# Optimization experiments

Measured on AMD Instinct MI355X. Metric: run time of the kernel, lower is better.

## Reference

```python
import jax, jax.numpy as jnp
import numpy as np

B, C, N, L, K, PRED = 64, 2, 1024, 24, 3, 12


def setup_inputs() -> dict:
    key = jax.random.key(0)
    ks = jax.random.split(key, 32)
    u = lambda k, shape, s: jax.random.uniform(k, shape, jnp.float32, -s, s)
    stdv_gc = 1.0 / np.sqrt(N)
    stdv_g = 1.0 / np.sqrt(N * (K + 1))
    stdv_r = 1.0 / np.sqrt(2 * N)
    inp = {
        'inputs': jax.random.normal(ks[0], (B, C, N, L), jnp.float32),
        'adj': (jax.random.uniform(ks[1], (N, N)) < 0.05).astype(jnp.float32),
        'gc_w': u(ks[2], (K, N, N), stdv_gc),
        'Wf': u(ks[3], (N, N * (K + 1)), stdv_g), 'bf': u(ks[4], (N,), stdv_g),
        'Wi': u(ks[5], (N, N * (K + 1)), stdv_g), 'bi': u(ks[6], (N,), stdv_g),
        'Wo': u(ks[7], (N, N * (K + 1)), stdv_g), 'bo': u(ks[8], (N,), stdv_g),
        'Wc': u(ks[9], (N, N * (K + 1)), stdv_g), 'bc': u(ks[10], (N,), stdv_g),
        'rWf': u(ks[11], (N, 2 * N), stdv_r), 'rbf': u(ks[12], (N,), stdv_r),
        'rWi': u(ks[13], (N, 2 * N), stdv_r), 'rbi': u(ks[14], (N,), stdv_r),
        'rWo': u(ks[15], (N, 2 * N), stdv_r), 'rbo': u(ks[16], (N,), stdv_r),
        'rWc': u(ks[17], (N, 2 * N), stdv_r), 'rbc': u(ks[18], (N,), stdv_r),
        'neighbor_w': u(ks[19], (N,), stdv_gc),
        'c': jnp.ones((1,), jnp.float32),
        'conv_w': u(ks[20], (C * PRED, C), 1.0 / np.sqrt(C)),
        'conv_b': u(ks[21], (C * PRED,), 1.0 / np.sqrt(C)),
    }
    return inp


def _build_A_list(adj, k):
    # tmp = sum(A, 0); zeros -> 1e-5; 'D_inverse' = diag(tmp) (as in original code)
    tmp = jnp.sum(adj, 0)
    tmp = jnp.where(tmp == 0, 1e-5, tmp)
    a_norm = tmp[:, None] * adj  # diag(tmp) @ A
    a_list = []
    a_tmp = jnp.eye(adj.shape[0], dtype=adj.dtype)
    for _ in range(k):
        a_tmp = jnp.minimum(a_tmp @ a_norm, 1.0)  # clamp max=1.0
        a_list.append(a_tmp)
    return a_list


def _forward(adj, inputs, gc_w, Wf, bf, Wi, bi, Wo, bo, Wc, bc,
             rWf, rbf, rWi, rbi, rWo, rbo, rWc, rbc, neighbor_w, c, conv_w, conv_b):
    b, ch, n, l = inputs.shape
    k = gc_w.shape[0]
    a_list = _build_A_list(adj, k)
    a_stack = jnp.stack(a_list)            # (K,N,N)
    eff_w = a_stack * gc_w                 # masked FilterLinear weights
    nbr = a_list[-1] @ neighbor_w          # (N,)
    Wg = jnp.concatenate([Wf, Wi, Wo, Wc], 0)      # fused gate weights (4N, (K+1)N)
    bg = jnp.concatenate([bf, bi, bo, bc], 0)
    rWg = jnp.concatenate([rWf, rWi, rWo, rWc], 0)  # (4N, 2N)
    rbg = jnp.concatenate([rbf, rbi, rbo, rbc], 0)

    def step(carry, x):  # x: (B,C,N)
        H, Cs, rH, rCs, _ = carry
        # gc = cat_k FilterLinear_k(x), each x @ (A_k*W_k)^T
        gc = jnp.einsum('bcn,kmn->bckm', x, eff_w).reshape(b, ch, k * n)
        g = jnp.concatenate([gc, H], -1) @ Wg.T + bg
        f, i, o, Ct = jnp.split(g, 4, -1)
        Cs = jax.nn.sigmoid(f) * (Cs * nbr) + jax.nn.sigmoid(i) * jnp.tanh(Ct)
        H = jax.nn.sigmoid(o) * jnp.tanh(Cs)
        rg = jnp.concatenate([x, rH], -1) @ rWg.T + rbg
        rf, ri, ro, rCt = jnp.split(rg, 4, -1)
        rCs = jax.nn.sigmoid(rf) * rCs + jax.nn.sigmoid(ri) * jnp.tanh(rCt)
        rH = jax.nn.sigmoid(ro) * jnp.tanh(rCs)
        var1 = jnp.var(x, axis=(0, 2), keepdims=True, ddof=1)   # (1,C,1), unbiased like torch
        var2 = jnp.var(gc, axis=(0, 2), keepdims=True, ddof=1)
        pred = (H * var1 * c + rH * var2) / (var1 + var2 * c)
        return (H, Cs, rH, rCs, pred), None

    z = jnp.zeros((b, ch, n), inputs.dtype)
    xs = jnp.moveaxis(inputs, -1, 0)  # (L,B,C,N)
    (H, Cs, rH, rCs, pred), _ = jax.lax.scan(step, (z, z, z, z, z), xs)
    # Conv1d(C, C*pred_len, k=1) then reshape (B,C,N,pred_len)
    out = jnp.einsum('bcn,oc->bon', pred, conv_w) + conv_b[:, None]
    return out.reshape(b, ch, n, -1)


def reference(inputs, adj, gc_w, Wf, bf, Wi, bi, Wo, bo, Wc, bc,
              rWf, rbf, rWi, rbi, rWo, rbo, rWc, rbc, neighbor_w, c, conv_w, conv_b):
    return _forward(adj, inputs, gc_w, Wf, bf, Wi, bi, Wo, bo, Wc, bc,
                    rWf, rbf, rWi, rbi, rWo, rbo, rWc, rbc, neighbor_w, c, conv_w, conv_b)
```

## Files before the change

kernel.cpp:

```cpp
#include <hip/hip_runtime.h>
#include <cmath>

#define NN 1024
#define BC 128
#define LS 24

typedef unsigned short u16;
typedef __attribute__((ext_vector_type(4))) float f32x4;
typedef __attribute__((ext_vector_type(8))) short bf16x8;
typedef __attribute__((ext_vector_type(8))) unsigned short u16x8;

typedef __attribute__((address_space(1))) const void* as1cv;
typedef __attribute__((address_space(3))) void* as3v;

#define GLD16(gp, lp) __builtin_amdgcn_global_load_lds((as1cv)(gp), (as3v)(lp), 16, 0, 0)

__device__ __forceinline__ float sigf(float x){ return 1.0f/(1.0f+expf(-x)); }

__device__ __forceinline__ u16 f2b(float x){
  union { float f; unsigned u; } v; v.f = x;
  unsigned r = v.u + 0x7FFFu + ((v.u >> 16) & 1u);
  return (u16)(r >> 16);
}
__device__ __forceinline__ float b2f(u16 b){
  union { unsigned u; float f; } v; v.u = ((unsigned)b) << 16;
  return v.f;
}

__global__ void k_prep(const float* __restrict__ inputs, const float* __restrict__ adj,
                       const float* __restrict__ Wf, const float* __restrict__ Wi,
                       const float* __restrict__ Wo, const float* __restrict__ Wc,
                       const float* __restrict__ rWf, const float* __restrict__ rWi,
                       const float* __restrict__ rWo, const float* __restrict__ rWc,
                       const float* __restrict__ bf_, const float* __restrict__ bi_,
                       const float* __restrict__ bo_, const float* __restrict__ bc_,
                       const float* __restrict__ rbf, const float* __restrict__ rbi,
                       const float* __restrict__ rbo, const float* __restrict__ rbc,
                       u16* __restrict__ Xb, float* __restrict__ csum,
                       u16* __restrict__ Wgxb, u16* __restrict__ WgHp,
                       u16* __restrict__ rWgxb, u16* __restrict__ rWgHp,
                       float* __restrict__ bgcat){
  int b = blockIdx.x, tid = threadIdx.x;
  if (b < 512){
    int idx = b*256 + tid;
    const float4* p = (const float4*)(inputs + (size_t)idx*LS);
    float v[LS];
    #pragma unroll
    for (int q = 0; q < 6; ++q){
      float4 f = p[q];
      v[q*4]=f.x; v[q*4+1]=f.y; v[q*4+2]=f.z; v[q*4+3]=f.w;
    }
    #pragma unroll
    for (int t = 0; t < LS; ++t)
      Xb[(size_t)t*BC*NN + idx] = f2b(v[t]);
  } else if (b < 576){
    int bb = b - 512;
    for (int j = tid; j < 1024; j += 256){
      float s = 0.f;
      for (int i = 0; i < 16; ++i) s += adj[(size_t)(bb*16+i)*1024 + j];
      csum[(size_t)bb*1024 + j] = s;
    }
  } else if (b < 592){
    int idx = (b-576)*256 + tid;
    int seg = idx >> 10, j = idx & 1023;
    bgcat[idx]      = (seg==0?bf_: seg==1?bi_: seg==2?bo_:bc_)[j];
    bgcat[4096+idx] = (seg==0?rbf: seg==1?rbi: seg==2?rbo:rbc)[j];
  } else {
    int idx = (b-592)*256 + tid;
    if (idx < 2097152){
      int kg = idx & 511, r = idx >> 9;
      int seg = r >> 10, j = r & 1023;
      const float* W = (seg==0?Wf: seg==1?Wi: seg==2?Wo:Wc) + (size_t)j*4096 + kg*8;
      float4 a = *(const float4*)W;
      float4 c = *(const float4*)(W + 4);
      u16x8 o = { f2b(a.x), f2b(a.y), f2b(a.z), f2b(a.w),
                  f2b(c.x), f2b(c.y), f2b(c.z), f2b(c.w) };
      if (kg < 384) *(u16x8*)(Wgxb + (size_t)r*3072 + kg*8) = o;
      else {
        int p = (j>>3)*32 + seg*8 + (j&7);
        *(u16x8*)(WgHp + (size_t)p*1024 + (kg*8 - 3072)) = o;
      }
    } else {
      int g2 = idx - 2097152;
      int kg = g2 & 255, r = g2 >> 8;
      int seg = r >> 10, j = r & 1023;
      const float* W = (seg==0?rWf: seg==1?rWi: seg==2?rWo:rWc) + (size_t)j*2048 + kg*8;
      float4 a = *(const float4*)W;
      float4 c = *(const float4*)(W + 4);
      u16x8 o = { f2b(a.x), f2b(a.y), f2b(a.z), f2b(a.w),
                  f2b(c.x), f2b(c.y), f2b(c.z), f2b(c.w) };
      if (kg < 128) *(u16x8*)(rWgxb + (size_t)r*1024 + kg*8) = o;
      else {
        int p = (j>>3)*32 + seg*8 + (j&7);
        *(u16x8*)(rWgHp + (size_t)p*1024 + (kg*8 - 1024)) = o;
      }
    }
  }
}

__global__ void k_colsum2(const float* __restrict__ part, float* __restrict__ tmp){
  int j = blockIdx.x*256 + threadIdx.x;
  float s = 0.f;
  for (int b = 0; b < 64; ++b) s += part[(size_t)b*1024 + j];
  tmp[j] = (s == 0.f) ? 1e-5f : s;
}

__global__ void k_anormT(const float* __restrict__ adj, const float* __restrict__ tmp,
                         u16* __restrict__ A1b, u16* __restrict__ anormT){
  __shared__ u16 t[64][65];
  int bi = blockIdx.y*64, bj = blockIdx.x*64;
  for (int e = threadIdx.x; e < 4096; e += 256){
    int r = e >> 6, cc = e & 63;
    float v = tmp[bi+r]*adj[(size_t)(bi+r)*1024 + bj+cc];
    A1b[(size_t)(bi+r)*1024 + bj+cc] = f2b(fminf(v, 1.f));
    t[r][cc] = f2b(v);
  }
  __syncthreads();
  for (int e = threadIdx.x; e < 4096; e += 256){
    int r = e >> 6, cc = e & 63;
    anormT[(size_t)(bj+r)*1024 + bi+cc] = t[cc][r];
  }
}

__global__ void k_nbr(const u16* __restrict__ A3b, const float* __restrict__ nw,
                      float* __restrict__ nbr){
  __shared__ float red[256];
  int row = blockIdx.x;
  float s = 0.f;
  for (int j = threadIdx.x; j < 1024; j += 256)
    s += b2f(A3b[(size_t)row*1024 + j])*nw[j];
  red[threadIdx.x] = s; __syncthreads();
  for (int st = 128; st > 0; st >>= 1){
    if (threadIdx.x < st) red[threadIdx.x] += red[threadIdx.x+st];
    __syncthreads();
  }
  if (threadIdx.x == 0) nbr[row] = red[0];
}

__global__ void k_effT(const u16* __restrict__ Ap, const float* __restrict__ gcw,
                       u16* __restrict__ effb, u16* __restrict__ effbT){
  __shared__ u16 t[64][65];
  int bi = blockIdx.y*64, bj = blockIdx.x*64;
  for (int e = threadIdx.x; e < 4096; e += 256){
    int r = e >> 6, cc = e & 63;
    size_t idx = (size_t)(bi+r)*1024 + bj+cc;
    u16 v = f2b(b2f(Ap[idx]) * gcw[idx]);
    effb[idx] = v;
    t[r][cc] = v;
  }
  __syncthreads();
  for (int e = threadIdx.x; e < 4096; e += 256){
    int r = e >> 6, cc = e & 63;
    effbT[(size_t)(bj+r)*3072 + bi+cc] = t[cc][r];
  }
}

__device__ __forceinline__ void mfma_tile(
    const u16* __restrict__ A, const u16* __restrict__ Bw, int K,
    const float* __restrict__ bias,
    float* __restrict__ outf, u16* __restrict__ outb, int ldc,
    u16* ldsA, u16* ldsB)
{
  const int tid  = threadIdx.x;
  const int lane = tid & 63;
  const int w    = tid >> 6;
  const int wr   = (w >> 1) * 64;
  const int wc   = (w & 1) * 64;
  f32x4 acc[4][4] = {};

  const int lrow = lane >> 3;
  const int srck = ((lane & 7) ^ lrow) * 8;
  for (int k0 = 0; k0 < K; k0 += 64){
    #pragma unroll
    for (int c = 0; c < 4; ++c){
      int row = w*32 + c*8;
      GLD16(A  + (size_t)(row + lrow)*K + k0 + srck, &ldsA[row*64]);
      GLD16(Bw + (size_t)(row + lrow)*K + k0 + srck, &ldsB[row*64]);
    }
    __syncthreads();
    #pragma unroll
    for (int kk = 0; kk < 2; ++kk) {
      bf16x8 af[4], bfr[4];
      #pragma unroll
      for (int mi = 0; mi < 4; ++mi) {
        int row = wr + mi*16 + (lane & 15);
        int grp = (kk*4 + (lane >> 4)) ^ (row & 7);
        af[mi] = *(const bf16x8*)&ldsA[row*64 + grp*8];
      }
      #pragma unroll
      for (int ni = 0; ni < 4; ++ni) {
        int row = wc + ni*16 + (lane & 15);
        int grp = (kk*4 + (lane >> 4)) ^ (row & 7);
        bfr[ni] = *(const bf16x8*)&ldsB[row*64 + grp*8];
      }
      #pragma unroll
      for (int mi = 0; mi < 4; ++mi)
        #pragma unroll
        for (int ni = 0; ni < 4; ++ni)
          acc[mi][ni] = __builtin_amdgcn_mfma_f32_16x16x32_bf16(af[mi], bfr[ni], acc[mi][ni], 0, 0, 0);
    }
    __syncthreads();
  }
  #pragma unroll
  for (int mi = 0; mi < 4; ++mi) {
    #pragma unroll
    for (int ni = 0; ni < 4; ++ni) {
      int col = wc + ni*16 + (lane & 15);
      #pragma unroll
      for (int q = 0; q < 4; ++q) {
        int row = wr + mi*16 + (lane >> 4)*4 + q;
        float v = acc[mi][ni][q];
        if (bias) v += bias[col];
        if (outf) outf[(size_t)row*ldc + col] = v;
        if (outb) outb[(size_t)row*ldc + col] = f2b(v);
      }
    }
  }
}

__global__ __launch_bounds__(256) void k_mfma_pre(
    const u16* __restrict__ Xb, const u16* __restrict__ Bcat,
    const float* __restrict__ bgcat, u16* __restrict__ prebuf)
{
  __shared__ u16 lds[16384];
  int id = blockIdx.y*64 + blockIdx.x;
  int bx = (id & 7)*8 + ((id >> 3) & 7);
  int by = id >> 6;
  mfma_tile(Xb + (size_t)by*128*1024, Bcat + (size_t)bx*128*1024, 1024,
            bgcat + bx*128, nullptr,
            prebuf + (size_t)by*128*8192 + bx*128, 8192,
            lds, lds + 8192);
}

__global__ __launch_bounds__(256) void k_mfma64(
    const u16* __restrict__ Ag, const u16* __restrict__ Bg, int K,
    int clamp1, int swz, u16* __restrict__ outb, int ldc)
{
  __shared__ u16 ldsA[64*128];
  __shared__ u16 ldsB[64*128];
  const int tid  = threadIdx.x;
  const int lane = tid & 63;
  const int w    = tid >> 6;
  const int wr   = (w >> 1) * 32;
  const int wc   = (w & 1) * 32;
  int bx = blockIdx.x, by = blockIdx.y;
  if (swz){
    int id = by*16 + bx;
    by = (id & 7)*8 + ((id >> 3) & 7);
    bx = id >> 6;
  }
  const u16* A = Ag + (size_t)by*64*K;
  const u16* B = Bg + (size_t)bx*64*K;
  f32x4 acc[2][2] = {};

  const int r4  = lane >> 4;
  const int g16 = lane & 15;
  for (int k0 = 0; k0 < K; k0 += 128){
    #pragma unroll
    for (int c = 0; c < 4; ++c){
      int rowb = w*16 + c*4;
      int row = rowb + r4;
      int srcg = (g16 & 8) | ((g16 & 7) ^ (row & 7));
      GLD16(A + (size_t)row*K + k0 + srcg*8, &ldsA[rowb*128]);
      GLD16(B + (size_t)row*K + k0 + srcg*8, &ldsB[rowb*128]);
    }
    __syncthreads();
    #pragma unroll
    for (int kk = 0; kk < 4; ++kk){
      int idx = kk*4 + (lane >> 4);
      bf16x8 af[2], bfr[2];
      #pragma unroll
      for (int mi = 0; mi < 2; ++mi){
        int row = wr + mi*16 + (lane & 15);
        int pa = (idx & 8) | ((idx & 7) ^ (row & 7));
        af[mi] = *(const bf16x8*)&ldsA[row*128 + pa*8];
      }
      #pragma unroll
      for (int ni = 0; ni < 2; ++ni){
        int row = wc + ni*16 + (lane & 15);
        int pb = (idx & 8) | ((idx & 7) ^ (row & 7));
        bfr[ni] = *(const bf16x8*)&ldsB[row*128 + pb*8];
      }
      #pragma unroll
      for (int mi = 0; mi < 2; ++mi)
        #pragma unroll
        for (int ni = 0; ni < 2; ++ni)
          acc[mi][ni] = __builtin_amdgcn_mfma_f32_16x16x32_bf16(af[mi], bfr[ni], acc[mi][ni], 0, 0, 0);
    }
    __syncthreads();
  }
  #pragma unroll
  for (int mi = 0; mi < 2; ++mi){
    #pragma unroll
    for (int ni = 0; ni < 2; ++ni){
      int col = bx*64 + wc + ni*16 + (lane & 15);
      #pragma unroll
      for (int q = 0; q < 4; ++q){
        int row = by*64 + wr + mi*16 + (lane >> 4)*4 + q;
        float v = acc[mi][ni][q];
        if (clamp1) v = fminf(v, 1.f);
        outb[(size_t)row*ldc + col] = f2b(v);
      }
    }
  }
}

__global__ __launch_bounds__(256) void k_step(
    const u16* __restrict__ WgHp, const u16* __restrict__ rWgHp,
    const u16* __restrict__ pre_t,
    const float* __restrict__ nbrv,
    u16* __restrict__ Hb2, u16* __restrict__ rHb2,
    float* __restrict__ Cs, float* __restrict__ rCs,
    float* __restrict__ Hf, float* __restrict__ rHf,
    int ph, int last)
{
  __shared__ u16 ldsA[2][64*128];
  __shared__ u16 ldsB[2][32*128];

  const int tid  = threadIdx.x;
  const int lane = tid & 63;
  const int w    = tid >> 6;
  const int bid  = blockIdx.x;
  const int job  = bid >> 8;
  const int rem  = bid & 255;
  const int s    = rem >> 1;
  const int r0   = (rem & 1) * 64;

  const u16* Bp   = (job ? rWgHp : WgHp) + (size_t)s*32*1024;
  const u16* Ab   = (job ? rHb2 : Hb2) + (size_t)ph*BC*NN + (size_t)r0*NN;
  const u16* pret = pre_t + (size_t)job*4096;
  u16* Hnext  = (job ? rHb2 : Hb2) + (size_t)(ph^1)*BC*NN;
  float* Csb  = job ? rCs : Cs;
  float* Hfin = job ? rHf : Hf;

  const int r4  = lane >> 4;
  const int g16 = lane & 15;

  auto STAGE = [&](int ck, int buf){
    int k0 = ck*128;
    #pragma unroll
    for (int c = 0; c < 4; ++c){
      int rowb = w*16 + c*4;
      int row = rowb + r4;
      int srcg = (g16 & 8) | ((g16 & 7) ^ (row & 7));
      GLD16(Ab + (size_t)row*1024 + k0 + srcg*8, &ldsA[buf][rowb*128]);
    }
    #pragma unroll
    for (int c = 0; c < 2; ++c){
      int rowb = w*8 + c*4;
      int row = rowb + r4;
      int srcg = (g16 & 8) | ((g16 & 7) ^ (row & 7));
      GLD16(Bp + (size_t)row*1024 + k0 + srcg*8, &ldsB[buf][rowb*128]);
    }
  };

  f32x4 acc[2] = {};
  STAGE(0, 0);
  #pragma unroll
  for (int t = 0; t < 8; ++t){
    const int cur = t & 1;
    if (t < 7){
      STAGE(t+1, cur^1);
      asm volatile("s_waitcnt vmcnt(6)" ::: "memory");
    } else {
      asm volatile("s_waitcnt vmcnt(0)" ::: "memory");
    }
    __builtin_amdgcn_sched_barrier(0);
    __builtin_amdgcn_s_barrier();
    #pragma unroll
    for (int kk = 0; kk < 4; ++kk){
      int idx = kk*4 + (lane >> 4);
      int rowa = w*16 + (lane & 15);
      int pa = (idx & 8) | ((idx & 7) ^ (rowa & 7));
      bf16x8 af = *(const bf16x8*)&ldsA[cur][rowa*128 + pa*8];
      #pragma unroll
      for (int ni = 0; ni < 2; ++ni){
        int rowb2 = ni*16 + (lane & 15);
        int pb = (idx & 8) | ((idx & 7) ^ (rowb2 & 7));
        bf16x8 bv = *(const bf16x8*)&ldsB[cur][rowb2*128 + pb*8];
        acc[ni] = __builtin_amdgcn_mfma_f32_16x16x32_bf16(af, bv, acc[ni], 0, 0, 0);
      }
    }
    __builtin_amdgcn_sched_barrier(0);
    __builtin_amdgcn_s_barrier();
  }

  #pragma unroll
  for (int ni = 0; ni < 2; ++ni){
    int pcol = ni*16 + (lane & 15);
    int gcol = (pcol >> 3)*1024 + s*8 + (pcol & 7);
    #pragma unroll
    for (int q = 0; q < 4; ++q){
      int row = r0 + w*16 + (lane >> 4)*4 + q;
      acc[ni][q] += b2f(pret[(size_t)row*8192 + gcol]);
    }
  }
  const bool act = (lane & 15) < 8;
  const int  c   = lane & 7;
  const int  col = s*8 + c;
  float fac = 1.f;
  if (!job && act) fac = nbrv[col];
  #pragma unroll
  for (int q = 0; q < 4; ++q){
    float a0 = acc[0][q], a1 = acc[1][q];
    float p1 = __shfl_xor(a0, 8);
    float p3 = __shfl_xor(a1, 8);
    if (act){
      int row = r0 + w*16 + (lane >> 4)*4 + q;
      float fg = sigf(a0), ig = sigf(p1), og = sigf(a1), ct = tanhf(p3);
      size_t cidx = (size_t)row*NN + col;
      float cs = fg*Csb[cidx]*fac + ig*ct;
      Csb[cidx] = cs;
      float h = og*tanhf(cs);
      Hnext[cidx] = f2b(h);
      if (last) Hfin[cidx] = h;
    }
  }
}

__global__ void k_var1(const u16* __restrict__ Xl, const u16* __restrict__ gcl,
                       float* __restrict__ part){
  int ch = blockIdx.x & 1, seg = blockIdx.x >> 1;
  int tid = threadIdx.x;
  float s1=0.f,q1=0.f,s2=0.f,q2=0.f;
  for (int bb = 0; bb < 2; ++bb){
    int row = (seg*2+bb)*2 + ch;
    const u16* xr = Xl + (size_t)row*1024;
    for (int n = tid; n < 1024; n += 256){ float v = b2f(xr[n]); s1 += v; q1 += v*v; }
    const u16* gr = gcl + (size_t)row*3072;
    for (int n = tid; n < 3072; n += 256){ float v = b2f(gr[n]); s2 += v; q2 += v*v; }
  }
  __shared__ float red[256][4];
  red[tid][0]=s1; red[tid][1]=q1; red[tid][2]=s2; red[tid][3]=q2;
  __syncthreads();
  for (int st = 128; st > 0; st >>= 1){
    if (tid < st){ for (int z = 0; z < 4; ++z) red[tid][z] += red[tid+st][z]; }
    __syncthreads();
  }
  if (tid == 0){ for (int z = 0; z < 4; ++z) part[(size_t)blockIdx.x*4 + z] = red[0][z]; }
}

__global__ void k_out(const float* __restrict__ H, const float* __restrict__ rH,
                      const float* __restrict__ part, const float* __restrict__ cptr,
                      const float* __restrict__ cw, const float* __restrict__ cb,
                      float* __restrict__ out){
  __shared__ float vsh[4];
  int tid = threadIdx.x;
  if (tid < 4){
    int ch = tid & 1, which = tid >> 1;
    float s = 0.f, q = 0.f;
    for (int seg = 0; seg < 32; ++seg){
      const float* p = part + (size_t)(seg*2+ch)*4 + which*2;
      s += p[0]; q += p[1];
    }
    float n = which ? 196608.f : 65536.f;
    vsh[tid] = (q - s*s/n) / (n - 1.f);
  }
  __syncthreads();
  int idx = blockIdx.x*256 + tid;
  int n = idx & 1023, b = idx >> 10;
  float c0 = cptr[0];
  float v10 = vsh[0], v11 = vsh[1], v20 = vsh[2], v21 = vsh[3];
  size_t i0 = (size_t)(b*2+0)*1024 + n, i1 = (size_t)(b*2+1)*1024 + n;
  float p0 = (H[i0]*v10*c0 + rH[i0]*v20) / (v10 + v20*c0);
  float p1 = (H[i1]*v11*c0 + rH[i1]*v21) / (v11 + v21*c0);
  float* ob = out + (size_t)b*24*1024 + n;
  #pragma unroll
  for (int o = 0; o < 24; ++o)
    ob[(size_t)o*1024] = p0*cw[o*2+0] + p1*cw[o*2+1] + cb[o];
}

extern "C" void kernel_launch(void* const* d_in, const int* in_sizes, int n_in,
                              void* d_out, int out_size, void* d_ws, size_t ws_size,
                              hipStream_t stream) {
  const float* inputs = (const float*)d_in[0];
  const float* adj    = (const float*)d_in[1];
  const float* gcw    = (const float*)d_in[2];
  const float* Wf  = (const float*)d_in[3];  const float* bf_ = (const float*)d_in[4];
  const float* Wi  = (const float*)d_in[5];  const float* bi_ = (const float*)d_in[6];
  const float* Wo  = (const float*)d_in[7];  const float* bo_ = (const float*)d_in[8];
  const float* Wc  = (const float*)d_in[9];  const float* bc_ = (const float*)d_in[10];
  const float* rWf = (const float*)d_in[11]; const float* rbf = (const float*)d_in[12];
  const float* rWi = (const float*)d_in[13]; const float* rbi = (const float*)d_in[14];
  const float* rWo = (const float*)d_in[15]; const float* rbo = (const float*)d_in[16];
  const float* rWc = (const float*)d_in[17]; const float* rbc = (const float*)d_in[18];
  const float* nw     = (const float*)d_in[19];
  const float* cscal  = (const float*)d_in[20];
  const float* convw  = (const float*)d_in[21];
  const float* convb  = (const float*)d_in[22];
  float* out = (float*)d_out;

  char* cur = (char*)d_ws;
  auto alloc = [&](size_t bytes) -> void* {
    void* p = cur; cur += (bytes + 255) & ~(size_t)255; return p;
  };
  u16*   Xb     = (u16*)  alloc((size_t)LS*BC*NN*2);
  float* csum   = (float*)alloc((size_t)64*1024*4);
  float* tmpv   = (float*)alloc(1024*4);
  u16*   anormT = (u16*)  alloc((size_t)NN*NN*2);
  u16*   Apowb  = (u16*)  alloc((size_t)3*NN*NN*2);
  float* nbrv   = (float*)alloc(1024*4);
  u16*   effb   = (u16*)  alloc((size_t)3*NN*NN*2);
  u16*   effbT  = (u16*)  alloc((size_t)3*NN*NN*2);
  u16*   Wgxb   = (u16*)  alloc((size_t)4096*3072*2);
  u16*   WgHp   = (u16*)  alloc((size_t)4096*1024*2);
  u16*   rWgHp  = (u16*)  alloc((size_t)4096*1024*2);
  u16*   Bcat   = (u16*)  alloc((size_t)8192*1024*2);
  float* bgcat  = (float*)alloc(8192*4);
  u16*   gclb   = (u16*)  alloc((size_t)BC*3072*2);
  u16*   prebuf = (u16*)  alloc((size_t)3072*8192*2);
  char*  zbase  = cur;
  u16*   Hb2    = (u16*)  alloc((size_t)2*BC*NN*2);
  u16*   rHb2   = (u16*)  alloc((size_t)2*BC*NN*2);
  float* Cs     = (float*)alloc((size_t)BC*NN*4);
  float* rCs    = (float*)alloc((size_t)BC*NN*4);
  size_t zlen   = (size_t)(cur - zbase);
  float* Hfv    = (float*)alloc((size_t)BC*NN*4);
  float* rHfv   = (float*)alloc((size_t)BC*NN*4);
  float* part   = (float*)alloc(64*4*4);

  u16* A1b = Apowb;
  u16* A2b = Apowb + (size_t)NN*NN;
  u16* A3b = Apowb + (size_t)2*NN*NN;
  u16* Cwb   = Bcat;
  u16* rWgxb = Bcat + (size_t)4096*1024;

  k_prep<<<592 + (2097152+1048576)/256, 256, 0, stream>>>(
      inputs, adj, Wf, Wi, Wo, Wc, rWf, rWi, rWo, rWc,
      bf_, bi_, bo_, bc_, rbf, rbi, rbo, rbc,
      Xb, csum, Wgxb, WgHp, rWgxb, rWgHp, bgcat);
  k_colsum2<<<4, 256, 0, stream>>>(csum, tmpv);
  dim3 g16(16, 16);
  k_anormT<<<g16, 256, 0, stream>>>(adj, tmpv, A1b, anormT);
  k_mfma64<<<g16, 256, 0, stream>>>(A1b, anormT, 1024, 1, 0, A2b, 1024);
  k_mfma64<<<g16, 256, 0, stream>>>(A2b, anormT, 1024, 1, 0, A3b, 1024);
  k_nbr<<<NN, 256, 0, stream>>>(A3b, nw, nbrv);
  dim3 geff(16, 48);
  k_effT<<<geff, 256, 0, stream>>>(Apowb, gcw, effb, effbT);

  dim3 gcwg(16, 64);
  k_mfma64<<<gcwg, 256, 0, stream>>>(Wgxb, effbT, 3072, 0, 1, Cwb, 1024);
  dim3 gpre(64, 24);
  k_mfma_pre<<<gpre, 256, 0, stream>>>(Xb, Bcat, bgcat, prebuf);
  dim3 ggcl(48, 2);
  k_mfma64<<<ggcl, 256, 0, stream>>>(Xb + (size_t)(LS-1)*BC*NN, effb, 1024, 0, 0, gclb, 3072);

  hipMemsetAsync(zbase, 0, zlen, stream);

  for (int t = 0; t < LS; ++t)
    k_step<<<512, 256, 0, stream>>>(WgHp, rWgHp,
        prebuf + (size_t)t*BC*8192,
        nbrv, Hb2, rHb2, Cs, rCs, Hfv, rHfv, t & 1, t == LS-1);

  k_var1<<<64, 256, 0, stream>>>(Xb + (size_t)(LS-1)*BC*NN, gclb, part);
  k_out<<<(64*1024)/256, 256, 0, stream>>>(Hfv, rHfv, part, cscal, convw, convb, out);
}
```

Baseline: 529.3 us.

## Fuse recurrent steps into one persistent kernel with grid barrier

```diff
diff --git a/kernel.cpp b/kernel.cpp
--- a/kernel.cpp
+++ b/kernel.cpp
@@ -4,6 +4,7 @@
 #define NN 1024
 #define BC 128
 #define LS 24
+#define LOOPBLK 256
 
 typedef unsigned short u16;
 typedef __attribute__((ext_vector_type(4))) float f32x4;
@@ -305,116 +306,147 @@
   }
 }
 
-__global__ __launch_bounds__(256) void k_step(
+__global__ __launch_bounds__(256) void k_loop(
     const u16* __restrict__ WgHp, const u16* __restrict__ rWgHp,
-    const u16* __restrict__ pre_t,
+    const u16* __restrict__ prebuf,
     const float* __restrict__ nbrv,
     u16* __restrict__ Hb2, u16* __restrict__ rHb2,
-    float* __restrict__ Cs, float* __restrict__ rCs,
     float* __restrict__ Hf, float* __restrict__ rHf,
-    int ph, int last)
+    int* __restrict__ bar)
 {
-  __shared__ u16 ldsA[2][64*128];
-  __shared__ u16 ldsB[2][32*128];
+  __shared__ u16 ldsB[32*1024];
+  __shared__ u16 ldsA[2][128*128];
 
   const int tid  = threadIdx.x;
   const int lane = tid & 63;
   const int w    = tid >> 6;
   const int bid  = blockIdx.x;
-  const int job  = bid >> 8;
-  const int rem  = bid & 255;
-  const int s    = rem >> 1;
-  const int r0   = (rem & 1) * 64;
+  const int job  = bid >> 7;
+  const int s    = bid & 127;
 
   const u16* Bp   = (job ? rWgHp : WgHp) + (size_t)s*32*1024;
-  const u16* Ab   = (job ? rHb2 : Hb2) + (size_t)ph*BC*NN + (size_t)r0*NN;
-  const u16* pret = pre_t + (size_t)job*4096;
-  u16* Hnext  = (job ? rHb2 : Hb2) + (size_t)(ph^1)*BC*NN;
-  float* Csb  = job ? rCs : Cs;
-  float* Hfin = job ? rHf : Hf;
+  const u16* Hsrc = job ? rHb2 : Hb2;
+  u16* Hdst       = job ? rHb2 : Hb2;
+  float* Hfin     = job ? rHf : Hf;
+  const u16* pre0 = prebuf + (size_t)job*4096;
 
   const int r4  = lane >> 4;
   const int g16 = lane & 15;
 
-  auto STAGE = [&](int ck, int buf){
-    int k0 = ck*128;
-    #pragma unroll
-    for (int c = 0; c < 4; ++c){
-      int rowb = w*16 + c*4;
-      int row = rowb + r4;
-      int srcg = (g16 & 8) | ((g16 & 7) ^ (row & 7));
-      GLD16(Ab + (size_t)row*1024 + k0 + srcg*8, &ldsA[buf][rowb*128]);
-    }
+  #pragma unroll
+  for (int ck = 0; ck < 8; ++ck){
     #pragma unroll
     for (int c = 0; c < 2; ++c){
       int rowb = w*8 + c*4;
       int row = rowb + r4;
       int srcg = (g16 & 8) | ((g16 & 7) ^ (row & 7));
-      GLD16(Bp + (size_t)row*1024 + k0 + srcg*8, &ldsB[buf][rowb*128]);
-    }
-  };
-
-  f32x4 acc[2] = {};
-  STAGE(0, 0);
-  #pragma unroll
-  for (int t = 0; t < 8; ++t){
-    const int cur = t & 1;
-    if (t < 7){
-      STAGE(t+1, cur^1);
-      asm volatile("s_waitcnt vmcnt(6)" ::: "memory");
-    } else {
-      asm volatile("s_waitcnt vmcnt(0)" ::: "memory");
-    }
-    __builtin_amdgcn_sched_barrier(0);
-    __builtin_amdgcn_s_barrier();
-    #pragma unroll
-    for (int kk = 0; kk < 4; ++kk){
-      int idx = kk*4 + (lane >> 4);
-      int rowa = w*16 + (lane & 15);
-      int pa = (idx & 8) | ((idx & 7) ^ (rowa & 7));
-      bf16x8 af = *(const bf16x8*)&ldsA[cur][rowa*128 + pa*8];
-      #pragma unroll
-      for (int ni = 0; ni < 2; ++ni){
-        int rowb2 = ni*16 + (lane & 15);
-        int pb = (idx & 8) | ((idx & 7) ^ (rowb2 & 7));
-        bf16x8 bv = *(const bf16x8*)&ldsB[cur][rowb2*128 + pb*8];
-        acc[ni] = __builtin_amdgcn_mfma_f32_16x16x32_bf16(af, bv, acc[ni], 0, 0, 0);
-      }
-    }
-    __builtin_amdgcn_sched_barrier(0);
-    __builtin_amdgcn_s_barrier();
-  }
-
-  #pragma unroll
-  for (int ni = 0; ni < 2; ++ni){
-    int pcol = ni*16 + (lane & 15);
-    int gcol = (pcol >> 3)*1024 + s*8 + (pcol & 7);
-    #pragma unroll
-    for (int q = 0; q < 4; ++q){
-      int row = r0 + w*16 + (lane >> 4)*4 + q;
-      acc[ni][q] += b2f(pret[(size_t)row*8192 + gcol]);
-    }
-  }
+      GLD16(Bp + (size_t)row*1024 + ck*128 + srcg*8, &ldsB[(ck*32 + rowb)*128]);
+    }
+  }
+
   const bool act = (lane & 15) < 8;
   const int  c   = lane & 7;
   const int  col = s*8 + c;
   float fac = 1.f;
   if (!job && act) fac = nbrv[col];
-  #pragma unroll
-  for (int q = 0; q < 4; ++q){
-    float a0 = acc[0][q], a1 = acc[1][q];
-    float p1 = __shfl_xor(a0, 8);
-    float p3 = __shfl_xor(a1, 8);
-    if (act){
-      int row = r0 + w*16 + (lane >> 4)*4 + q;
-      float fg = sigf(a0), ig = sigf(p1), og = sigf(a1), ct = tanhf(p3);
-      size_t cidx = (size_t)row*NN + col;
-      float cs = fg*Csb[cidx]*fac + ig*ct;
-      Csb[cidx] = cs;
-      float h = og*tanhf(cs);
-      Hnext[cidx] = f2b(h);
-      if (last) Hfin[cidx] = h;
-    }
+  float csr[2][4] = {};
+
+  asm volatile("s_waitcnt vmcnt(0)" ::: "memory");
+  __syncthreads();
+
+  for (int t = 0; t < LS; ++t){
+    const int ph = t & 1;
+    const u16* Ab   = Hsrc + (size_t)ph*BC*NN;
+    const u16* pret = pre0 + (size_t)t*BC*8192;
+    u16* Hnext      = Hdst + (size_t)(ph^1)*BC*NN;
+
+    float preld[2][2][4];
+    #pragma unroll
+    for (int mi = 0; mi < 2; ++mi)
+      #pragma unroll
+      for (int ni = 0; ni < 2; ++ni){
+        int pcol = ni*16 + (lane & 15);
+        int gcol = (pcol >> 3)*1024 + s*8 + (pcol & 7);
+        #pragma unroll
+        for (int q = 0; q < 4; ++q){
+          int row = w*32 + mi*16 + (lane >> 4)*4 + q;
+          preld[mi][ni][q] = b2f(pret[(size_t)row*8192 + gcol]);
+        }
+      }
+
+    auto STAGEA = [&](int ck, int buf){
+      int k0 = ck*128;
+      #pragma unroll
+      for (int cc = 0; cc < 8; ++cc){
+        int rowb = w*32 + cc*4;
+        int row = rowb + r4;
+        int srcg = (g16 & 8) | ((g16 & 7) ^ (row & 7));
+        GLD16(Ab + (size_t)row*1024 + k0 + srcg*8, &ldsA[buf][rowb*128]);
+      }
+    };
+
+    f32x4 acc[2][2] = {};
+    STAGEA(0, 0);
+    #pragma unroll
+    for (int ck = 0; ck < 8; ++ck){
+      const int cur = ck & 1;
+      if (ck < 7){
+        STAGEA(ck+1, cur^1);
+        asm volatile("s_waitcnt vmcnt(8)" ::: "memory");
+      } else {
+        asm volatile("s_waitcnt vmcnt(0)" ::: "memory");
+      }
+      __builtin_amdgcn_sched_barrier(0);
+      __builtin_amdgcn_s_barrier();
+      #pragma unroll
+      for (int kk = 0; kk < 4; ++kk){
+        int idx = kk*4 + (lane >> 4);
+        #pragma unroll
+        for (int mi = 0; mi < 2; ++mi){
+          int rowa = w*32 + mi*16 + (lane & 15);
+          int pa = (idx & 8) | ((idx & 7) ^ (rowa & 7));
+          bf16x8 af = *(const bf16x8*)&ldsA[cur][rowa*128 + pa*8];
+          #pragma unroll
+          for (int ni = 0; ni < 2; ++ni){
+            int rowb2 = ni*16 + (lane & 15);
+            int pb = (idx & 8) | ((idx & 7) ^ (rowb2 & 7));
+            bf16x8 bv = *(const bf16x8*)&ldsB[(ck*32 + rowb2)*128 + pb*8];
+            acc[mi][ni] = __builtin_amdgcn_mfma_f32_16x16x32_bf16(af, bv, acc[mi][ni], 0, 0, 0);
+          }
+        }
+      }
+      __builtin_amdgcn_sched_barrier(0);
+      __builtin_amdgcn_s_barrier();
+    }
+
+    #pragma unroll
+    for (int mi = 0; mi < 2; ++mi){
+      #pragma unroll
+      for (int q = 0; q < 4; ++q){
+        float a0 = acc[mi][0][q] + preld[mi][0][q];
+        float a1 = acc[mi][1][q] + preld[mi][1][q];
+        float p1 = __shfl_xor(a0, 8);
+        float p3 = __shfl_xor(a1, 8);
+        if (act){
+          int row = w*32 + mi*16 + (lane >> 4)*4 + q;
+          float fg = sigf(a0), ig = sigf(p1), og = sigf(a1), ct = tanhf(p3);
+          float cs = fg*csr[mi][q]*fac + ig*ct;
+          csr[mi][q] = cs;
+          float h = og*tanhf(cs);
+          Hnext[(size_t)row*NN + col] = f2b(h);
+          if (t == LS-1) Hfin[(size_t)row*NN + col] = h;
+        }
+      }
+    }
+
+    __threadfence();
+    __syncthreads();
+    if (tid == 0){
+      atomicAdd(&bar[t], 1);
+      while (__hip_atomic_load(&bar[t], __ATOMIC_RELAXED, __HIP_MEMORY_SCOPE_AGENT) < LOOPBLK) {}
+    }
+    __syncthreads();
+    __threadfence();
   }
 }
 
@@ -512,8 +544,7 @@
   char*  zbase  = cur;
   u16*   Hb2    = (u16*)  alloc((size_t)2*BC*NN*2);
   u16*   rHb2   = (u16*)  alloc((size_t)2*BC*NN*2);
-  float* Cs     = (float*)alloc((size_t)BC*NN*4);
-  float* rCs    = (float*)alloc((size_t)BC*NN*4);
+  int*   bar    = (int*)  alloc(LS*4);
   size_t zlen   = (size_t)(cur - zbase);
   float* Hfv    = (float*)alloc((size_t)BC*NN*4);
   float* rHfv   = (float*)alloc((size_t)BC*NN*4);
@@ -547,10 +578,8 @@
 
   hipMemsetAsync(zbase, 0, zlen, stream);
 
-  for (int t = 0; t < LS; ++t)
-    k_step<<<512, 256, 0, stream>>>(WgHp, rWgHp,
-        prebuf + (size_t)t*BC*8192,
-        nbrv, Hb2, rHb2, Cs, rCs, Hfv, rHfv, t & 1, t == LS-1);
+  k_loop<<<LOOPBLK, 256, 0, stream>>>(WgHp, rWgHp, prebuf, nbrv,
+                                      Hb2, rHb2, Hfv, rHfv, bar);
 
   k_var1<<<64, 256, 0, stream>>>(Xb + (size_t)(LS-1)*BC*NN, gclb, part);
   k_out<<<(64*1024)/256, 256, 0, stream>>>(Hfv, rHfv, part, cscal, convw, convb, out);
```

Result: slower. 1.541 ms (+191.2%).

## Merge small prep kernels and widen recurrent step tiles to 512 threads

Applied to the files above, without the earlier changes.

```diff
diff --git a/kernel.cpp b/kernel.cpp
--- a/kernel.cpp
+++ b/kernel.cpp
@@ -122,36 +122,39 @@
   }
 }
 
-__global__ void k_nbr(const u16* __restrict__ A3b, const float* __restrict__ nw,
-                      float* __restrict__ nbr){
+__global__ void k_nbreff(const u16* __restrict__ A3b, const float* __restrict__ nw,
+                         float* __restrict__ nbr,
+                         const u16* __restrict__ Ap, const float* __restrict__ gcw,
+                         u16* __restrict__ effb, u16* __restrict__ effbT){
   __shared__ float red[256];
-  int row = blockIdx.x;
-  float s = 0.f;
-  for (int j = threadIdx.x; j < 1024; j += 256)
-    s += b2f(A3b[(size_t)row*1024 + j])*nw[j];
-  red[threadIdx.x] = s; __syncthreads();
-  for (int st = 128; st > 0; st >>= 1){
-    if (threadIdx.x < st) red[threadIdx.x] += red[threadIdx.x+st];
+  __shared__ u16 t[64][65];
+  int b = blockIdx.x, tid = threadIdx.x;
+  if (b < 1024){
+    int row = b;
+    float s = 0.f;
+    for (int j = tid; j < 1024; j += 256)
+      s += b2f(A3b[(size_t)row*1024 + j])*nw[j];
+    red[tid] = s; __syncthreads();
+    for (int st = 128; st > 0; st >>= 1){
+      if (tid < st) red[tid] += red[tid+st];
+      __syncthreads();
+    }
+    if (tid == 0) nbr[row] = red[0];
+  } else {
+    int e2 = b - 1024;
+    int bj = (e2 & 15)*64, bi = (e2 >> 4)*64;
+    for (int e = tid; e < 4096; e += 256){
+      int r = e >> 6, cc = e & 63;
+      size_t idx = (size_t)(bi+r)*1024 + bj+cc;
+      u16 v = f2b(b2f(Ap[idx]) * gcw[idx]);
+      effb[idx] = v;
+      t[r][cc] = v;
+    }
     __syncthreads();
-  }
-  if (threadIdx.x == 0) nbr[row] = red[0];
-}
-
-__global__ void k_effT(const u16* __restrict__ Ap, const float* __restrict__ gcw,
-                       u16* __restrict__ effb, u16* __restrict__ effbT){
-  __shared__ u16 t[64][65];
-  int bi = blockIdx.y*64, bj = blockIdx.x*64;
-  for (int e = threadIdx.x; e < 4096; e += 256){
-    int r = e >> 6, cc = e & 63;
-    size_t idx = (size_t)(bi+r)*1024 + bj+cc;
-    u16 v = f2b(b2f(Ap[idx]) * gcw[idx]);
-    effb[idx] = v;
-    t[r][cc] = v;
-  }
-  __syncthreads();
-  for (int e = threadIdx.x; e < 4096; e += 256){
-    int r = e >> 6, cc = e & 63;
-    effbT[(size_t)(bj+r)*3072 + bi+cc] = t[cc][r];
+    for (int e = tid; e < 4096; e += 256){
+      int r = e >> 6, cc = e & 63;
+      effbT[(size_t)(bj+r)*3072 + bi+cc] = t[cc][r];
+    }
   }
 }
 
@@ -220,16 +223,26 @@
 
 __global__ __launch_bounds__(256) void k_mfma_pre(
     const u16* __restrict__ Xb, const u16* __restrict__ Bcat,
-    const float* __restrict__ bgcat, u16* __restrict__ prebuf)
+    const float* __restrict__ bgcat, u16* __restrict__ prebuf,
+    const u16* __restrict__ Xlast, const u16* __restrict__ effb,
+    u16* __restrict__ gclb)
 {
   __shared__ u16 lds[16384];
-  int id = blockIdx.y*64 + blockIdx.x;
-  int bx = (id & 7)*8 + ((id >> 3) & 7);
-  int by = id >> 6;
-  mfma_tile(Xb + (size_t)by*128*1024, Bcat + (size_t)bx*128*1024, 1024,
-            bgcat + bx*128, nullptr,
-            prebuf + (size_t)by*128*8192 + bx*128, 8192,
-            lds, lds + 8192);
+  int id = blockIdx.x;
+  if (id < 1536){
+    int bx = (id & 7)*8 + ((id >> 3) & 7);
+    int by = id >> 6;
+    mfma_tile(Xb + (size_t)by*128*1024, Bcat + (size_t)bx*128*1024, 1024,
+              bgcat + bx*128, nullptr,
+              prebuf + (size_t)by*128*8192 + bx*128, 8192,
+              lds, lds + 8192);
+  } else {
+    int g = id - 1536;
+    mfma_tile(Xlast, effb + (size_t)g*128*1024, 1024,
+              nullptr, nullptr,
+              gclb + (size_t)g*128, 3072,
+              lds, lds + 8192);
+  }
 }
 
 __global__ __launch_bounds__(256) void k_mfma64(
@@ -305,7 +318,7 @@
   }
 }
 
-__global__ __launch_bounds__(256) void k_step(
+__global__ __launch_bounds__(512) void k_step(
     const u16* __restrict__ WgHp, const u16* __restrict__ rWgHp,
     const u16* __restrict__ pre_t,
     const float* __restrict__ nbrv,
@@ -315,18 +328,20 @@
     int ph, int last)
 {
   __shared__ u16 ldsA[2][64*128];
-  __shared__ u16 ldsB[2][32*128];
+  __shared__ u16 ldsB[2][64*128];
 
   const int tid  = threadIdx.x;
   const int lane = tid & 63;
   const int w    = tid >> 6;
+  const int mw   = w >> 1;
+  const int nh   = w & 1;
   const int bid  = blockIdx.x;
-  const int job  = bid >> 8;
-  const int rem  = bid & 255;
-  const int s    = rem >> 1;
+  const int job  = bid >> 7;
+  const int rem  = bid & 127;
+  const int p    = rem >> 1;
   const int r0   = (rem & 1) * 64;
 
-  const u16* Bp   = (job ? rWgHp : WgHp) + (size_t)s*32*1024;
+  const u16* Bp   = (job ? rWgHp : WgHp) + (size_t)p*64*1024;
   const u16* Ab   = (job ? rHb2 : Hb2) + (size_t)ph*BC*NN + (size_t)r0*NN;
   const u16* pret = pre_t + (size_t)job*4096;
   u16* Hnext  = (job ? rHb2 : Hb2) + (size_t)(ph^1)*BC*NN;
@@ -339,17 +354,11 @@
   auto STAGE = [&](int ck, int buf){
     int k0 = ck*128;
     #pragma unroll
-    for (int c = 0; c < 4; ++c){
-      int rowb = w*16 + c*4;
-      int row = rowb + r4;
-      int srcg = (g16 & 8) | ((g16 & 7) ^ (row & 7));
-      GLD16(Ab + (size_t)row*1024 + k0 + srcg*8, &ldsA[buf][rowb*128]);
-    }
-    #pragma unroll
     for (int c = 0; c < 2; ++c){
       int rowb = w*8 + c*4;
       int row = rowb + r4;
       int srcg = (g16 & 8) | ((g16 & 7) ^ (row & 7));
+      GLD16(Ab + (size_t)row*1024 + k0 + srcg*8, &ldsA[buf][rowb*128]);
       GLD16(Bp + (size_t)row*1024 + k0 + srcg*8, &ldsB[buf][rowb*128]);
     }
   };
@@ -361,7 +370,7 @@
     const int cur = t & 1;
     if (t < 7){
       STAGE(t+1, cur^1);
-      asm volatile("s_waitcnt vmcnt(6)" ::: "memory");
+      asm volatile("s_waitcnt vmcnt(4)" ::: "memory");
     } else {
       asm volatile("s_waitcnt vmcnt(0)" ::: "memory");
     }
@@ -370,12 +379,12 @@
     #pragma unroll
     for (int kk = 0; kk < 4; ++kk){
       int idx = kk*4 + (lane >> 4);
-      int rowa = w*16 + (lane & 15);
+      int rowa = mw*16 + (lane & 15);
       int pa = (idx & 8) | ((idx & 7) ^ (rowa & 7));
       bf16x8 af = *(const bf16x8*)&ldsA[cur][rowa*128 + pa*8];
       #pragma unroll
       for (int ni = 0; ni < 2; ++ni){
-        int rowb2 = ni*16 + (lane & 15);
+        int rowb2 = nh*32 + ni*16 + (lane & 15);
         int pb = (idx & 8) | ((idx & 7) ^ (rowb2 & 7));
         bf16x8 bv = *(const bf16x8*)&ldsB[cur][rowb2*128 + pb*8];
         acc[ni] = __builtin_amdgcn_mfma_f32_16x16x32_bf16(af, bv, acc[ni], 0, 0, 0);
@@ -385,29 +394,22 @@
     __builtin_amdgcn_s_barrier();
   }
 
-  #pragma unroll
-  for (int ni = 0; ni < 2; ++ni){
-    int pcol = ni*16 + (lane & 15);
-    int gcol = (pcol >> 3)*1024 + s*8 + (pcol & 7);
-    #pragma unroll
-    for (int q = 0; q < 4; ++q){
-      int row = r0 + w*16 + (lane >> 4)*4 + q;
-      acc[ni][q] += b2f(pret[(size_t)row*8192 + gcol]);
-    }
-  }
+  const int b8 = (lane & 15) >> 3;
+  const int gcol0 = (0*2 + b8)*1024 + (2*p + nh)*8 + (lane & 7);
+  const int gcol1 = (1*2 + b8)*1024 + (2*p + nh)*8 + (lane & 7);
   const bool act = (lane & 15) < 8;
-  const int  c   = lane & 7;
-  const int  col = s*8 + c;
+  const int  col = p*16 + nh*8 + (lane & 7);
   float fac = 1.f;
   if (!job && act) fac = nbrv[col];
   #pragma unroll
   for (int q = 0; q < 4; ++q){
-    float a0 = acc[0][q], a1 = acc[1][q];
-    float p1 = __shfl_xor(a0, 8);
-    float p3 = __shfl_xor(a1, 8);
+    int row = r0 + mw*16 + (lane >> 4)*4 + q;
+    float a0 = acc[0][q] + b2f(pret[(size_t)row*8192 + gcol0]);
+    float a1 = acc[1][q] + b2f(pret[(size_t)row*8192 + gcol1]);
+    float vi  = __shfl_xor(a0, 8);
+    float vct = __shfl_xor(a1, 8);
     if (act){
-      int row = r0 + w*16 + (lane >> 4)*4 + q;
-      float fg = sigf(a0), ig = sigf(p1), og = sigf(a1), ct = tanhf(p3);
+      float fg = sigf(a0), ig = sigf(vi), og = sigf(a1), ct = tanhf(vct);
       size_t cidx = (size_t)row*NN + col;
       float cs = fg*Csb[cidx]*fac + ig*ct;
       Csb[cidx] = cs;
@@ -529,26 +531,21 @@
       inputs, adj, Wf, Wi, Wo, Wc, rWf, rWi, rWo, rWc,
       bf_, bi_, bo_, bc_, rbf, rbi, rbo, rbc,
       Xb, csum, Wgxb, WgHp, rWgxb, rWgHp, bgcat);
+  hipMemsetAsync(zbase, 0, zlen, stream);
   k_colsum2<<<4, 256, 0, stream>>>(csum, tmpv);
   dim3 g16(16, 16);
   k_anormT<<<g16, 256, 0, stream>>>(adj, tmpv, A1b, anormT);
   k_mfma64<<<g16, 256, 0, stream>>>(A1b, anormT, 1024, 1, 0, A2b, 1024);
   k_mfma64<<<g16, 256, 0, stream>>>(A2b, anormT, 1024, 1, 0, A3b, 1024);
-  k_nbr<<<NN, 256, 0, stream>>>(A3b, nw, nbrv);
-  dim3 geff(16, 48);
-  k_effT<<<geff, 256, 0, stream>>>(Apowb, gcw, effb, effbT);
+  k_nbreff<<<1792, 256, 0, stream>>>(A3b, nw, nbrv, Apowb, gcw, effb, effbT);
 
   dim3 gcwg(16, 64);
   k_mfma64<<<gcwg, 256, 0, stream>>>(Wgxb, effbT, 3072, 0, 1, Cwb, 1024);
-  dim3 gpre(64, 24);
-  k_mfma_pre<<<gpre, 256, 0, stream>>>(Xb, Bcat, bgcat, prebuf);
-  dim3 ggcl(48, 2);
-  k_mfma64<<<ggcl, 256, 0, stream>>>(Xb + (size_t)(LS-1)*BC*NN, effb, 1024, 0, 0, gclb, 3072);
-
-  hipMemsetAsync(zbase, 0, zlen, stream);
+  k_mfma_pre<<<1560, 256, 0, stream>>>(Xb, Bcat, bgcat, prebuf,
+                                       Xb + (size_t)(LS-1)*BC*NN, effb, gclb);
 
   for (int t = 0; t < LS; ++t)
-    k_step<<<512, 256, 0, stream>>>(WgHp, rWgHp,
+    k_step<<<256, 512, 0, stream>>>(WgHp, rWgHp,
         prebuf + (size_t)t*BC*8192,
         nbrv, Hb2, rHb2, Cs, rCs, Hfv, rHfv, t & 1, t == LS-1);
 
```

Result: no change. 539.3 us (+1.9%).

## Fold per-timestep input projection GEMM into recurrent step kernel launches

Applied to the files above, without the earlier changes.

```diff
diff --git a/kernel.cpp b/kernel.cpp
--- a/kernel.cpp
+++ b/kernel.cpp
@@ -155,81 +155,80 @@
   }
 }
 
-__device__ __forceinline__ void mfma_tile(
-    const u16* __restrict__ A, const u16* __restrict__ Bw, int K,
-    const float* __restrict__ bias,
-    float* __restrict__ outf, u16* __restrict__ outb, int ldc,
-    u16* ldsA, u16* ldsB)
+__device__ __forceinline__ void pre_tile64(int g, const u16* __restrict__ Xs,
+                                           const u16* __restrict__ Bcat,
+                                           const float* __restrict__ bgcat,
+                                           u16* __restrict__ outs, u16* lds)
 {
+  u16* ldsA = lds;
+  u16* ldsB = lds + 8192;
   const int tid  = threadIdx.x;
   const int lane = tid & 63;
   const int w    = tid >> 6;
-  const int wr   = (w >> 1) * 64;
-  const int wc   = (w & 1) * 64;
-  f32x4 acc[4][4] = {};
-
-  const int lrow = lane >> 3;
-  const int srck = ((lane & 7) ^ lrow) * 8;
-  for (int k0 = 0; k0 < K; k0 += 64){
+  const int wr   = (w >> 1) * 32;
+  const int wc   = (w & 1) * 32;
+  const int rh = g >> 7, cp = g & 127;
+  const u16* A = Xs + (size_t)rh*64*1024;
+  const u16* B = Bcat + (size_t)cp*64*1024;
+  f32x4 acc[2][2] = {};
+
+  const int r4  = lane >> 4;
+  const int g16 = lane & 15;
+  for (int k0 = 0; k0 < 1024; k0 += 128){
     #pragma unroll
     for (int c = 0; c < 4; ++c){
-      int row = w*32 + c*8;
-      GLD16(A  + (size_t)(row + lrow)*K + k0 + srck, &ldsA[row*64]);
-      GLD16(Bw + (size_t)(row + lrow)*K + k0 + srck, &ldsB[row*64]);
+      int rowb = w*16 + c*4;
+      int row = rowb + r4;
+      int srcg = (g16 & 8) | ((g16 & 7) ^ (row & 7));
+      GLD16(A + (size_t)row*1024 + k0 + srcg*8, &ldsA[rowb*128]);
+      GLD16(B + (size_t)row*1024 + k0 + srcg*8, &ldsB[rowb*128]);
     }
     __syncthreads();
     #pragma unroll
-    for (int kk = 0; kk < 2; ++kk) {
-      bf16x8 af[4], bfr[4];
-      #pragma unroll
-      for (int mi = 0; mi < 4; ++mi) {
+    for (int kk = 0; kk < 4; ++kk){
+      int idx = kk*4 + (lane >> 4);
+      bf16x8 af[2], bfr[2];
+      #pragma unroll
+      for (int mi = 0; mi < 2; ++mi){
         int row = wr + mi*16 + (lane & 15);
-        int grp = (kk*4 + (lane >> 4)) ^ (row & 7);
-        af[mi] = *(const bf16x8*)&ldsA[row*64 + grp*8];
-      }
-      #pragma unroll
-      for (int ni = 0; ni < 4; ++ni) {
+        int pa = (idx & 8) | ((idx & 7) ^ (row & 7));
+        af[mi] = *(const bf16x8*)&ldsA[row*128 + pa*8];
+      }
+      #pragma unroll
+      for (int ni = 0; ni < 2; ++ni){
         int row = wc + ni*16 + (lane & 15);
-        int grp = (kk*4 + (lane >> 4)) ^ (row & 7);
-        bfr[ni] = *(const bf16x8*)&ldsB[row*64 + grp*8];
-      }
-      #pragma unroll
-      for (int mi = 0; mi < 4; ++mi)
+        int pb = (idx & 8) | ((idx & 7) ^ (row & 7));
+        bfr[ni] = *(const bf16x8*)&ldsB[row*128 + pb*8];
+      }
+      #pragma unroll
+      for (int mi = 0; mi < 2; ++mi)
         #pragma unroll
-        for (int ni = 0; ni < 4; ++ni)
+        for (int ni = 0; ni < 2; ++ni)
           acc[mi][ni] = __builtin_amdgcn_mfma_f32_16x16x32_bf16(af[mi], bfr[ni], acc[mi][ni], 0, 0, 0);
     }
     __syncthreads();
   }
   #pragma unroll
-  for (int mi = 0; mi < 4; ++mi) {
-    #pragma unroll
-    for (int ni = 0; ni < 4; ++ni) {
-      int col = wc + ni*16 + (lane & 15);
-      #pragma unroll
-      for (int q = 0; q < 4; ++q) {
-        int row = wr + mi*16 + (lane >> 4)*4 + q;
-        float v = acc[mi][ni][q];
-        if (bias) v += bias[col];
-        if (outf) outf[(size_t)row*ldc + col] = v;
-        if (outb) outb[(size_t)row*ldc + col] = f2b(v);
-      }
-    }
-  }
-}
-
-__global__ __launch_bounds__(256) void k_mfma_pre(
-    const u16* __restrict__ Xb, const u16* __restrict__ Bcat,
-    const float* __restrict__ bgcat, u16* __restrict__ prebuf)
+  for (int mi = 0; mi < 2; ++mi){
+    #pragma unroll
+    for (int ni = 0; ni < 2; ++ni){
+      int col = cp*64 + wc + ni*16 + (lane & 15);
+      float bv = bgcat[col];
+      #pragma unroll
+      for (int q = 0; q < 4; ++q){
+        int row = rh*64 + wr + mi*16 + (lane >> 4)*4 + q;
+        outs[(size_t)row*8192 + col] = f2b(acc[mi][ni][q] + bv);
+      }
+    }
+  }
+}
+
+__global__ __launch_bounds__(256) void k_pre0(
+    const u16* __restrict__ Xs, const u16* __restrict__ Bcat,
+    const float* __restrict__ bgcat, u16* __restrict__ outs)
 {
   __shared__ u16 lds[16384];
-  int id = blockIdx.y*64 + blockIdx.x;
-  int bx = (id & 7)*8 + ((id >> 3) & 7);
-  int by = id >> 6;
-  mfma_tile(Xb + (size_t)by*128*1024, Bcat + (size_t)bx*128*1024, 1024,
-            bgcat + bx*128, nullptr,
-            prebuf + (size_t)by*128*8192 + bx*128, 8192,
-            lds, lds + 8192);
+  pre_tile64(blockIdx.x, Xs, Bcat, bgcat, outs, lds);
 }
 
 __global__ __launch_bounds__(256) void k_mfma64(
@@ -308,19 +307,29 @@
 __global__ __launch_bounds__(256) void k_step(
     const u16* __restrict__ WgHp, const u16* __restrict__ rWgHp,
     const u16* __restrict__ pre_t,
+    const u16* __restrict__ Xb_next, const u16* __restrict__ Bcat,
+    const float* __restrict__ bgcat, u16* __restrict__ pre_next, int do_pre,
     const float* __restrict__ nbrv,
     u16* __restrict__ Hb2, u16* __restrict__ rHb2,
     float* __restrict__ Cs, float* __restrict__ rCs,
     float* __restrict__ Hf, float* __restrict__ rHf,
     int ph, int last)
 {
-  __shared__ u16 ldsA[2][64*128];
-  __shared__ u16 ldsB[2][32*128];
+  __shared__ u16 lds[24576];
 
   const int tid  = threadIdx.x;
   const int lane = tid & 63;
   const int w    = tid >> 6;
   const int bid  = blockIdx.x;
+
+  if (bid >= 512){
+    if (do_pre) pre_tile64(bid - 512, Xb_next, Bcat, bgcat, pre_next, lds);
+    return;
+  }
+
+  u16* ldsA0 = lds;
+  u16* ldsB0 = lds + 16384;
+
   const int job  = bid >> 8;
   const int rem  = bid & 255;
   const int s    = rem >> 1;
@@ -343,14 +352,14 @@
       int rowb = w*16 + c*4;
       int row = rowb + r4;
       int srcg = (g16 & 8) | ((g16 & 7) ^ (row & 7));
-      GLD16(Ab + (size_t)row*1024 + k0 + srcg*8, &ldsA[buf][rowb*128]);
+      GLD16(Ab + (size_t)row*1024 + k0 + srcg*8, &ldsA0[buf*8192 + rowb*128]);
     }
     #pragma unroll
     for (int c = 0; c < 2; ++c){
       int rowb = w*8 + c*4;
       int row = rowb + r4;
       int srcg = (g16 & 8) | ((g16 & 7) ^ (row & 7));
-      GLD16(Bp + (size_t)row*1024 + k0 + srcg*8, &ldsB[buf][rowb*128]);
+      GLD16(Bp + (size_t)row*1024 + k0 + srcg*8, &ldsB0[buf*4096 + rowb*128]);
     }
   };
 
@@ -372,12 +381,12 @@
       int idx = kk*4 + (lane >> 4);
       int rowa = w*16 + (lane & 15);
       int pa = (idx & 8) | ((idx & 7) ^ (rowa & 7));
-      bf16x8 af = *(const bf16x8*)&ldsA[cur][rowa*128 + pa*8];
+      bf16x8 af = *(const bf16x8*)&ldsA0[cur*8192 + rowa*128 + pa*8];
       #pragma unroll
       for (int ni = 0; ni < 2; ++ni){
         int rowb2 = ni*16 + (lane & 15);
         int pb = (idx & 8) | ((idx & 7) ^ (rowb2 & 7));
-        bf16x8 bv = *(const bf16x8*)&ldsB[cur][rowb2*128 + pb*8];
+        bf16x8 bv = *(const bf16x8*)&ldsB0[cur*4096 + rowb2*128 + pb*8];
         acc[ni] = __builtin_amdgcn_mfma_f32_16x16x32_bf16(af, bv, acc[ni], 0, 0, 0);
       }
     }
@@ -529,6 +538,7 @@
       inputs, adj, Wf, Wi, Wo, Wc, rWf, rWi, rWo, rWc,
       bf_, bi_, bo_, bc_, rbf, rbi, rbo, rbc,
       Xb, csum, Wgxb, WgHp, rWgxb, rWgHp, bgcat);
+  hipMemsetAsync(zbase, 0, zlen, stream);
   k_colsum2<<<4, 256, 0, stream>>>(csum, tmpv);
   dim3 g16(16, 16);
   k_anormT<<<g16, 256, 0, stream>>>(adj, tmpv, A1b, anormT);
@@ -540,17 +550,18 @@
 
   dim3 gcwg(16, 64);
   k_mfma64<<<gcwg, 256, 0, stream>>>(Wgxb, effbT, 3072, 0, 1, Cwb, 1024);
-  dim3 gpre(64, 24);
-  k_mfma_pre<<<gpre, 256, 0, stream>>>(Xb, Bcat, bgcat, prebuf);
+  k_pre0<<<256, 256, 0, stream>>>(Xb, Bcat, bgcat, prebuf);
   dim3 ggcl(48, 2);
   k_mfma64<<<ggcl, 256, 0, stream>>>(Xb + (size_t)(LS-1)*BC*NN, effb, 1024, 0, 0, gclb, 3072);
 
-  hipMemsetAsync(zbase, 0, zlen, stream);
-
-  for (int t = 0; t < LS; ++t)
-    k_step<<<512, 256, 0, stream>>>(WgHp, rWgHp,
+  for (int t = 0; t < LS; ++t){
+    int tn = (t+1 < LS) ? t+1 : t;
+    k_step<<<768, 256, 0, stream>>>(WgHp, rWgHp,
         prebuf + (size_t)t*BC*8192,
+        Xb + (size_t)tn*BC*NN, Bcat, bgcat,
+        prebuf + (size_t)tn*BC*8192, (t+1 < LS) ? 1 : 0,
         nbrv, Hb2, rHb2, Cs, rCs, Hfv, rHfv, t & 1, t == LS-1);
+  }
 
   k_var1<<<64, 256, 0, stream>>>(Xb + (size_t)(LS-1)*BC*NN, gclb, part);
   k_out<<<(64*1024)/256, 256, 0, stream>>>(Hfv, rHfv, part, cscal, convw, convb, out);
```

New measurement: 507.4 us, median of 2. 4.1% less time.
